# Performance work log

Measured on AMD Instinct MI355X. Metric: run time of the kernel, lower is better.

## Reference

```python
import jax, jax.numpy as jnp
import numpy as np

NU, NI = 100000, 50000          # num_users, num_items
N = NU + NI                      # total nodes
D = 64                           # hidden_dim
DE = 16                          # eigs_dim
L = 2                            # n_layers
E = 1500000                      # edges per layer
NP = 14                          # 2**(sample_hop+1)-2 path types
EPS = 1e-5


def setup_inputs() -> dict:
    key = jax.random.key(0)
    ks = jax.random.split(key, 7)
    return {
        "user_emb": jax.random.normal(ks[0], (NU, D), jnp.float32) * 0.1,
        "item_emb": jax.random.normal(ks[1], (NI, D), jnp.float32) * 0.1,
        "eigs": jax.random.normal(ks[2], (N, DE), jnp.float32),
        "lambda0": jax.random.normal(ks[3], (L,), jnp.float32) * 0.1,
        "path_w": jax.random.normal(ks[4], (L, NP), jnp.float32) * 0.1,
        "indices": jax.random.randint(ks[5], (L, 2, E), 0, N),
        "path_type": jax.random.randint(ks[6], (L, E), 0, NP),
    }


def _layer_norm(x):
    mu = x.mean(-1, keepdims=True)
    var = ((x - mu) ** 2).mean(-1, keepdims=True)
    return (x - mu) * jax.lax.rsqrt(var + EPS)


def _sparse_softmax(row, vals, n):
    # torch: clamp(exp(v), min=-5, max=5) -> effectively min(exp(v), 5)
    e = jnp.clip(jnp.exp(vals), -5.0, 5.0)
    s = jax.ops.segment_sum(e, row, num_segments=n)
    s = jnp.where(s == 0.0, 1.0, s)
    return e / s[row]


def _encoder(x, idx, pt, eigs, lam, pw):
    y = _layer_norm(x)                                   # [N, D]
    r, c = idx[0], idx[1]                                # [E]
    yc = y[c]                                            # [E, D]
    xs = (y[r] * yc).sum(-1) * (1.0 / jnp.sqrt(jnp.float32(D)))  # [E]
    ys = (eigs[r] * eigs[c]).sum(-1)                     # [E]
    s0 = _sparse_softmax(r, xs + jnp.exp(lam) * ys, N)
    s1 = _sparse_softmax(r, pw[pt], N)
    s = 0.5 * (s0 + s1)                                  # mean over the two scores
    # SpMM: out[r] += s_e * y[c_e]
    return jax.ops.segment_sum(s[:, None] * yc, r, num_segments=N)


def reference(user_emb, item_emb, eigs, lambda0, path_w, indices, path_type):
    x = jnp.concatenate([user_emb, item_emb], axis=0)    # [N, D]
    embs = [x]
    for l in range(L):
        x = _encoder(x, indices[l], path_type[l], eigs, lambda0[l], path_w[l])
        embs.append(x)
    return jnp.mean(jnp.stack(embs, axis=1), axis=1)      # [N, D]
```

## Files before the change

kernel.cpp:

```cpp
#include <hip/hip_runtime.h>
#include <hip/hip_bf16.h>

#define NUSERS 100000
#define NITEMS 50000
#define NN 150000
#define DD 64
#define DE 16
#define NE 1500000
#define NPATH 14
#define LN_EPS 1e-5f

#define BROWS 512
#define NBUK 293
#define NB (2 * NBUK)
#define CHUNK 4096
#define NCHUNK ((NE + CHUNK - 1) / CHUNK)
#define NCPB 2
#define NSC ((NCHUNK + NCPB - 1) / NCPB)
#define CAP 5888

#define EIGBLK ((NN * DE) / 256)

typedef float vf2 __attribute__((ext_vector_type(2)));

__device__ __forceinline__ vf2 unpk(unsigned u) {
    vf2 r;
    r.x = __uint_as_float(u << 16);
    r.y = __uint_as_float(u & 0xffff0000u);
    return r;
}
__device__ __forceinline__ unsigned f2b(float f) {
    union { float f; unsigned u; } v; v.f = f;
    return (v.u + 0x7fffu + ((v.u >> 16) & 1u)) >> 16;
}

template<int CTRL>
__device__ __forceinline__ float dppmov(float x) {
    return __int_as_float(
        __builtin_amdgcn_mov_dpp(__float_as_int(x), CTRL, 0xF, 0xF, true));
}

__device__ __forceinline__ int wscan(int v, int lane) {
    #pragma unroll
    for (int d = 1; d < 64; d <<= 1) {
        int u = __shfl_up(v, d, 64);
        v += (lane >= d) ? u : 0;
    }
    return v;
}

__global__ void k_init(int* __restrict__ curbuk) {
    int t = blockIdx.x * 256 + threadIdx.x;
    if (t < NB) curbuk[t] = t * CAP;
}

__global__ void k_eigln(const float* __restrict__ uemb,
                        const float* __restrict__ iemb,
                        const float* __restrict__ eigs,
                        unsigned short* __restrict__ e16,
                        unsigned short* __restrict__ y) {
    int blk = blockIdx.x;
    int t = threadIdx.x;
    if (blk < EIGBLK) {
        int i = blk * 256 + t;
        e16[i] = (unsigned short)f2b(eigs[i]);
    } else {
        int row = (blk - EIGBLK) * 4 + (t >> 6);
        int lane = t & 63;
        if (row >= NN) return;
        int i = row * DD + lane;
        float v = (row < NUSERS) ? uemb[i] : iemb[i - NUSERS * DD];
        float s = v;
        #pragma unroll
        for (int m = 32; m; m >>= 1) s += __shfl_xor(s, m, 64);
        float mu = s * (1.0f / 64.0f);
        float d = v - mu;
        float q = d * d;
        #pragma unroll
        for (int m = 32; m; m >>= 1) q += __shfl_xor(q, m, 64);
        float rs = rsqrtf(q * (1.0f / 64.0f) + LN_EPS);
        y[i] = (unsigned short)f2b(d * rs);
    }
}

__global__ __launch_bounds__(512) void k_pscatter(
        const int* __restrict__ idx,
        const int* __restrict__ ptyp,
        int* __restrict__ curbuk,
        unsigned int* __restrict__ stage) {
    int blk = blockIdx.x;
    int layer = blk / NSC;
    int kk = (blk - layer * NSC) * NCPB;
    __shared__ int h[NBUK];
    __shared__ int hofs[NBUK];
    for (int t = threadIdx.x; t < NBUK; t += 512) h[t] = 0;
    __syncthreads();
    const int* rrow = idx + (size_t)layer * 2 * NE;
    const int* ccol = rrow + NE;
    const int* pp   = ptyp + (size_t)layer * NE;
    int base = kk * CHUNK;
    int lim = min(NCPB * CHUNK, NE - base);
    for (int j = threadIdx.x; j < lim; j += 512)
        atomicAdd(&h[rrow[base + j] >> 9], 1);
    __syncthreads();
    for (int t = threadIdx.x; t < NBUK; t += 512) {
        int c = h[t];
        hofs[t] = c ? atomicAdd(&curbuk[layer * NBUK + t], c) : 0;
    }
    __syncthreads();
    for (int j = threadIdx.x; j < lim; j += 512) {
        int e = base + j;
        int r = rrow[e];
        int pos = atomicAdd(&hofs[r >> 9], 1);
        stage[pos] = (unsigned)ccol[e] | ((unsigned)pp[e] << 18)
                   | ((unsigned)(r & 511) << 22);
    }
}

__global__ __launch_bounds__(1024) void k_bscatter(
        const unsigned int* __restrict__ stage,
        const int* __restrict__ curbuk,
        int* __restrict__ csv,
        int2* __restrict__ roff) {
    __shared__ int scnt[BROWS];
    __shared__ int scur[BROWS];
    __shared__ int wsum[16];
    int b = blockIdx.x;
    int t = threadIdx.x;
    int lane = t & 63, w = t >> 6;
    int layer = b / NBUK;
    int brow0 = (b - layer * NBUK) * BROWS;
    int nrows = min(BROWS, NN - brow0);
    int start = b * CAP;
    int n = curbuk[b] - start;
    if (t < BROWS) scnt[t] = 0;
    __syncthreads();
    for (int p = t; p < n; p += 1024)
        atomicAdd(&scnt[stage[start + p] >> 22], 1);
    __syncthreads();
    int orig = (t < BROWS) ? scnt[t] : 0;
    int s = wscan(orig, lane);
    if (lane == 63) wsum[w] = s;
    __syncthreads();
    if (w == 0) {
        int x = (lane < 16) ? wsum[lane] : 0;
        #pragma unroll
        for (int d = 1; d < 16; d <<= 1) {
            int u = __shfl_up(x, d, 64);
            x += (lane >= d) ? u : 0;
        }
        if (lane < 16) wsum[lane] = x;
    }
    __syncthreads();
    int wb = (w > 0) ? wsum[w - 1] : 0;
    int excl = wb + s - orig;
    if (t < BROWS) {
        scur[t] = excl;
        if (t < nrows)
            roff[(size_t)layer * NN + brow0 + t] =
                make_int2(start + excl, start + excl + orig);
    }
    __syncthreads();
    for (int p = t; p < n; p += 1024) {
        unsigned rec = stage[start + p];
        int pos = atomicAdd(&scur[rec >> 22], 1);
        csv[start + pos] = (int)(rec & 0x3fffffu);
    }
}

__global__ void k_row(const unsigned short* __restrict__ y,
                      const unsigned short* __restrict__ e16,
                      const int2* __restrict__ roff,
                      const int* __restrict__ csv,
                      const float* __restrict__ pw,
                      const float* __restrict__ lam,
                      int layer, int row0,
                      const float* __restrict__ uemb,
                      const float* __restrict__ iemb,
                      float* __restrict__ x1,
                      unsigned short* __restrict__ y1,
                      float* __restrict__ out) {
    __shared__ float pexp[NPATH];
    __shared__ float selam;
    int t = threadIdx.x;
    if (t < NPATH) pexp[t] = fminf(expf(pw[layer * NPATH + t]), 5.0f);
    if (t == NPATH) selam = expf(lam[layer]);
    __syncthreads();

    int row = row0 + blockIdx.x * 4 + (t >> 6);
    int lane = t & 63;
    int g = lane >> 3;
    int sl = lane & 7;
    int2 pr = roff[row];
    int p0 = pr.x, p1 = pr.y;

    uint4 ar = reinterpret_cast<const uint4*>(y + (size_t)row * DD)[sl];
    vf2 a0 = unpk(ar.x), a1 = unpk(ar.y), a2 = unpk(ar.z), a3 = unpk(ar.w);
    unsigned eru = reinterpret_cast<const unsigned*>(e16 + (size_t)row * DE)[sl];
    vf2 er = unpk(eru);
    float elam = selam;

    float sum0 = 0.f, sum1 = 0.f;
    vf2 A0 = {0.f, 0.f}, A1 = {0.f, 0.f}, A2 = {0.f, 0.f}, A3 = {0.f, 0.f};
    vf2 B0 = {0.f, 0.f}, B1 = {0.f, 0.f}, B2 = {0.f, 0.f}, B3 = {0.f, 0.f};

    int pend = p0 + ((p1 - p0) & ~7);

    for (int p = p0; p < pend; p += 8) {
        int rec = csv[p + g];
        int c = rec & 0x3ffff;
        uint4 bv = reinterpret_cast<const uint4*>(y + (size_t)c * DD)[sl];
        unsigned ecu = reinterpret_cast<const unsigned*>(e16 + (size_t)c * DE)[sl];
        vf2 b0 = unpk(bv.x), b1 = unpk(bv.y), b2 = unpk(bv.z), b3 = unpk(bv.w);
        vf2 px = a0 * b0;
        px += a1 * b1;
        px += a2 * b2;
        px += a3 * b3;
        vf2 ec = unpk(ecu);
        vf2 tt = px * 0.125f + (er * ec) * elam;
        float sc = tt.x + tt.y;
        sc += dppmov<0xB1>(sc);
        sc += dppmov<0x4E>(sc);
        sc += dppmov<0x141>(sc);
        float e0 = fminf(__expf(sc), 5.0f);
        float e1 = pexp[(rec >> 18) & 0xF];
        sum0 += e0; sum1 += e1;
        A0 += e0 * b0; A1 += e0 * b1; A2 += e0 * b2; A3 += e0 * b3;
        B0 += e1 * b0; B1 += e1 * b1; B2 += e1 * b2; B3 += e1 * b3;
    }

    if (pend < p1) {
        int q = pend + g;
        int qc = (q < p1) ? q : (p1 - 1);
        int rec = csv[qc];
        int c = rec & 0x3ffff;
        uint4 bv = reinterpret_cast<const uint4*>(y + (size_t)c * DD)[sl];
        unsigned ecu = reinterpret_cast<const unsigned*>(e16 + (size_t)c * DE)[sl];
        vf2 b0 = unpk(bv.x), b1 = unpk(bv.y), b2 = unpk(bv.z), b3 = unpk(bv.w);
        vf2 px = a0 * b0;
        px += a1 * b1;
        px += a2 * b2;
        px += a3 * b3;
        vf2 ec = unpk(ecu);
        vf2 tt = px * 0.125f + (er * ec) * elam;
        float sc = tt.x + tt.y;
        sc += dppmov<0xB1>(sc);
        sc += dppmov<0x4E>(sc);
        sc += dppmov<0x141>(sc);
        bool ok = q < p1;
        float e0 = ok ? fminf(__expf(sc), 5.0f) : 0.f;
        float e1 = ok ? pexp[(rec >> 18) & 0xF] : 0.f;
        sum0 += e0; sum1 += e1;
        A0 += e0 * b0; A1 += e0 * b1; A2 += e0 * b2; A3 += e0 * b3;
        B0 += e1 * b0; B1 += e1 * b1; B2 += e1 * b2; B3 += e1 * b3;
    }

    sum0 += dppmov<0x128>(sum0);
    sum1 += dppmov<0x128>(sum1);
    #pragma unroll
    for (int m = 16; m <= 32; m <<= 1) {
        sum0 += __shfl_xor(sum0, m, 64);
        sum1 += __shfl_xor(sum1, m, 64);
    }
    float rinv0 = 0.5f / ((sum0 == 0.f) ? 1.f : sum0);
    float rinv1 = 0.5f / ((sum1 == 0.f) ? 1.f : sum1);

    vf2 o0 = rinv0 * A0 + rinv1 * B0, o1 = rinv0 * A1 + rinv1 * B1;
    vf2 o2 = rinv0 * A2 + rinv1 * B2, o3 = rinv0 * A3 + rinv1 * B3;
    o0.x += dppmov<0x128>(o0.x); o0.y += dppmov<0x128>(o0.y);
    o1.x += dppmov<0x128>(o1.x); o1.y += dppmov<0x128>(o1.y);
    o2.x += dppmov<0x128>(o2.x); o2.y += dppmov<0x128>(o2.y);
    o3.x += dppmov<0x128>(o3.x); o3.y += dppmov<0x128>(o3.y);
    #pragma unroll
    for (int m = 16; m <= 32; m <<= 1) {
        vf2 s;
        s.x = __shfl_xor(o0.x, m, 64); s.y = __shfl_xor(o0.y, m, 64); o0 += s;
        s.x = __shfl_xor(o1.x, m, 64); s.y = __shfl_xor(o1.y, m, 64); o1 += s;
        s.x = __shfl_xor(o2.x, m, 64); s.y = __shfl_xor(o2.y, m, 64); o2 += s;
        s.x = __shfl_xor(o3.x, m, 64); s.y = __shfl_xor(o3.y, m, 64); o3 += s;
    }
    if (g == 0) {
        int ofs = sl * 8;
        float v0 = o0.x, v1 = o0.y, v2 = o1.x, v3 = o1.y;
        float v4 = o2.x, v5 = o2.y, v6 = o3.x, v7 = o3.y;
        if (layer == 0) {
            float* dst = x1 + (size_t)row * DD + ofs;
            reinterpret_cast<float4*>(dst)[0] = make_float4(v0, v1, v2, v3);
            reinterpret_cast<float4*>(dst)[1] = make_float4(v4, v5, v6, v7);
            float s = v0+v1+v2+v3+v4+v5+v6+v7;
            s += __shfl_xor(s, 1, 64);
            s += __shfl_xor(s, 2, 64);
            s += __shfl_xor(s, 4, 64);
            float mu = s * (1.0f / 64.0f);
            float d0=v0-mu, d1=v1-mu, d2=v2-mu, d3=v3-mu;
            float d4=v4-mu, d5=v5-mu, d6=v6-mu, d7=v7-mu;
            float qv = d0*d0+d1*d1+d2*d2+d3*d3+d4*d4+d5*d5+d6*d6+d7*d7;
            qv += __shfl_xor(qv, 1, 64);
            qv += __shfl_xor(qv, 2, 64);
            qv += __shfl_xor(qv, 4, 64);
            float rs = rsqrtf(qv * (1.0f / 64.0f) + LN_EPS);
            uint4 pk;
            pk.x = f2b(d0*rs) | (f2b(d1*rs) << 16);
            pk.y = f2b(d2*rs) | (f2b(d3*rs) << 16);
            pk.z = f2b(d4*rs) | (f2b(d5*rs) << 16);
            pk.w = f2b(d6*rs) | (f2b(d7*rs) << 16);
            reinterpret_cast<uint4*>(y1 + (size_t)row * DD)[sl] = pk;
        } else {
            const float* e = (row < NUSERS)
                ? (uemb + (size_t)row * DD + ofs)
                : (iemb + (size_t)(row - NUSERS) * DD + ofs);
            const float* xp = x1 + (size_t)row * DD + ofs;
            float4 ea = reinterpret_cast<const float4*>(e)[0];
            float4 eb = reinterpret_cast<const float4*>(e)[1];
            float4 xa = reinterpret_cast<const float4*>(xp)[0];
            float4 xb = reinterpret_cast<const float4*>(xp)[1];
            float* dst = out + (size_t)row * DD + ofs;
            const float k3 = 1.0f / 3.0f;
            reinterpret_cast<float4*>(dst)[0] = make_float4(
                (ea.x + xa.x + v0) * k3, (ea.y + xa.y + v1) * k3,
                (ea.z + xa.z + v2) * k3, (ea.w + xa.w + v3) * k3);
            reinterpret_cast<float4*>(dst)[1] = make_float4(
                (eb.x + xb.x + v4) * k3, (eb.y + xb.y + v5) * k3,
                (eb.z + xb.z + v6) * k3, (eb.w + xb.w + v7) * k3);
        }
    }
}

extern "C" void kernel_launch(void* const* d_in, const int* in_sizes, int n_in,
                              void* d_out, int out_size, void* d_ws, size_t ws_size,
                              hipStream_t stream) {
    const float* uemb = (const float*)d_in[0];
    const float* iemb = (const float*)d_in[1];
    const float* eigs = (const float*)d_in[2];
    const float* lam  = (const float*)d_in[3];
    const float* pw   = (const float*)d_in[4];
    const int* idx    = (const int*)d_in[5];
    const int* ptyp   = (const int*)d_in[6];

    char* w = (char*)d_ws;
    unsigned int*   stage  = (unsigned int*)(w);
    float*          x1     = (float*)(w);
    unsigned short* y0     = (unsigned short*)(w + 38400000);
    unsigned short* y1     = (unsigned short*)(w + 57600000);
    int*            csv    = (int*)(w + 76800000);
    int2*           roff   = (int2*)(w + 90601472);
    unsigned short* e16    = (unsigned short*)(w + 93001472);
    int*            curbuk = (int*)(w + 97801472);

    k_init<<<3, 256, 0, stream>>>(curbuk);
    k_pscatter<<<2 * NSC, 512, 0, stream>>>(idx, ptyp, curbuk, stage);
    k_bscatter<<<NB, 1024, 0, stream>>>(stage, curbuk, csv, roff);

    const int gRows = NN / 4;
    k_eigln<<<EIGBLK + gRows, 256, 0, stream>>>(uemb, iemb, eigs, e16, y0);

    const int gH = NN / 8;
    for (int q = 0; q < 2; ++q)
        k_row<<<gH, 256, 0, stream>>>(y0, e16, roff, csv, pw, lam, 0,
                                      q * (NN / 2),
                                      nullptr, nullptr, x1, y1, nullptr);
    for (int q = 0; q < 2; ++q)
        k_row<<<gH, 256, 0, stream>>>(y1, e16, roff + NN, csv, pw, lam, 1,
                                      q * (NN / 2),
                                      uemb, iemb, x1, nullptr, (float*)d_out);
}
```

Measured before the change: 395.9 us.

## Use 1024-row buckets for CSR build and merge split row launches

The two-pass bucket sort that builds per-row edge lists now uses 1024-row buckets (147 per layer) instead of 512. The bucket scatter kernel uses all 1024 threads for row counts and prefix scan. The partition kernel goes back to one 4096-edge chunk per block, giving more blocks with fewer shared-memory histogram bins each. Each layer's row-aggregation kernel is now launched once over all rows instead of as two half launches, removing launch overhead. Larger buckets mean more atomic contention per bucket and a bigger per-bucket capacity in staging memory.

```diff
diff --git a/kernel.cpp b/kernel.cpp
--- a/kernel.cpp
+++ b/kernel.cpp
@@ -10,14 +10,12 @@
 #define NPATH 14
 #define LN_EPS 1e-5f
 
-#define BROWS 512
-#define NBUK 293
+#define BROWS 1024
+#define NBUK 147
 #define NB (2 * NBUK)
 #define CHUNK 4096
 #define NCHUNK ((NE + CHUNK - 1) / CHUNK)
-#define NCPB 2
-#define NSC ((NCHUNK + NCPB - 1) / NCPB)
-#define CAP 5888
+#define CAP 11264
 
 #define EIGBLK ((NN * DE) / 256)
 
@@ -89,8 +87,8 @@
         int* __restrict__ curbuk,
         unsigned int* __restrict__ stage) {
     int blk = blockIdx.x;
-    int layer = blk / NSC;
-    int kk = (blk - layer * NSC) * NCPB;
+    int layer = blk / NCHUNK;
+    int k = blk - layer * NCHUNK;
     __shared__ int h[NBUK];
     __shared__ int hofs[NBUK];
     for (int t = threadIdx.x; t < NBUK; t += 512) h[t] = 0;
@@ -98,10 +96,10 @@
     const int* rrow = idx + (size_t)layer * 2 * NE;
     const int* ccol = rrow + NE;
     const int* pp   = ptyp + (size_t)layer * NE;
-    int base = kk * CHUNK;
-    int lim = min(NCPB * CHUNK, NE - base);
+    int base = k * CHUNK;
+    int lim = min(CHUNK, NE - base);
     for (int j = threadIdx.x; j < lim; j += 512)
-        atomicAdd(&h[rrow[base + j] >> 9], 1);
+        atomicAdd(&h[rrow[base + j] >> 10], 1);
     __syncthreads();
     for (int t = threadIdx.x; t < NBUK; t += 512) {
         int c = h[t];
@@ -111,9 +109,9 @@
     for (int j = threadIdx.x; j < lim; j += 512) {
         int e = base + j;
         int r = rrow[e];
-        int pos = atomicAdd(&hofs[r >> 9], 1);
+        int pos = atomicAdd(&hofs[r >> 10], 1);
         stage[pos] = (unsigned)ccol[e] | ((unsigned)pp[e] << 18)
-                   | ((unsigned)(r & 511) << 22);
+                   | ((unsigned)(r & 1023) << 22);
     }
 }
 
@@ -133,12 +131,12 @@
     int nrows = min(BROWS, NN - brow0);
     int start = b * CAP;
     int n = curbuk[b] - start;
-    if (t < BROWS) scnt[t] = 0;
+    scnt[t] = 0;
     __syncthreads();
     for (int p = t; p < n; p += 1024)
         atomicAdd(&scnt[stage[start + p] >> 22], 1);
     __syncthreads();
-    int orig = (t < BROWS) ? scnt[t] : 0;
+    int orig = scnt[t];
     int s = wscan(orig, lane);
     if (lane == 63) wsum[w] = s;
     __syncthreads();
@@ -154,12 +152,10 @@
     __syncthreads();
     int wb = (w > 0) ? wsum[w - 1] : 0;
     int excl = wb + s - orig;
-    if (t < BROWS) {
-        scur[t] = excl;
-        if (t < nrows)
-            roff[(size_t)layer * NN + brow0 + t] =
-                make_int2(start + excl, start + excl + orig);
-    }
+    scur[t] = excl;
+    if (t < nrows)
+        roff[(size_t)layer * NN + brow0 + t] =
+            make_int2(start + excl, start + excl + orig);
     __syncthreads();
     for (int p = t; p < n; p += 1024) {
         unsigned rec = stage[start + p];
@@ -174,7 +170,7 @@
                       const int* __restrict__ csv,
                       const float* __restrict__ pw,
                       const float* __restrict__ lam,
-                      int layer, int row0,
+                      int layer,
                       const float* __restrict__ uemb,
                       const float* __restrict__ iemb,
                       float* __restrict__ x1,
@@ -187,7 +183,7 @@
     if (t == NPATH) selam = expf(lam[layer]);
     __syncthreads();
 
-    int row = row0 + blockIdx.x * 4 + (t >> 6);
+    int row = blockIdx.x * 4 + (t >> 6);
     int lane = t & 63;
     int g = lane >> 3;
     int sl = lane & 7;
@@ -347,20 +343,15 @@
     unsigned short* e16    = (unsigned short*)(w + 93001472);
     int*            curbuk = (int*)(w + 97801472);
 
-    k_init<<<3, 256, 0, stream>>>(curbuk);
-    k_pscatter<<<2 * NSC, 512, 0, stream>>>(idx, ptyp, curbuk, stage);
+    k_init<<<2, 256, 0, stream>>>(curbuk);
+    k_pscatter<<<2 * NCHUNK, 512, 0, stream>>>(idx, ptyp, curbuk, stage);
     k_bscatter<<<NB, 1024, 0, stream>>>(stage, curbuk, csv, roff);
 
     const int gRows = NN / 4;
     k_eigln<<<EIGBLK + gRows, 256, 0, stream>>>(uemb, iemb, eigs, e16, y0);
 
-    const int gH = NN / 8;
-    for (int q = 0; q < 2; ++q)
-        k_row<<<gH, 256, 0, stream>>>(y0, e16, roff, csv, pw, lam, 0,
-                                      q * (NN / 2),
-                                      nullptr, nullptr, x1, y1, nullptr);
-    for (int q = 0; q < 2; ++q)
-        k_row<<<gH, 256, 0, stream>>>(y1, e16, roff + NN, csv, pw, lam, 1,
-                                      q * (NN / 2),
-                                      uemb, iemb, x1, nullptr, (float*)d_out);
-}
+    k_row<<<gRows, 256, 0, stream>>>(y0, e16, roff, csv, pw, lam, 0,
+                                     nullptr, nullptr, x1, y1, nullptr);
+    k_row<<<gRows, 256, 0, stream>>>(y1, e16, roff + NN, csv, pw, lam, 1,
+                                     uemb, iemb, x1, nullptr, (float*)d_out);
+}
```

Result: faster. 384.3 us (-2.9%).
